# Kernel optimization log

Measured on AMD Instinct MI355X. Metric: run time of the kernel, lower is better.

## Reference

```python
import jax, jax.numpy as jnp
import numpy as np

B, D_IN, D_OUT, E = 8192, 1024, 1024, 16


def setup_inputs() -> dict:
    key = jax.random.key(0)
    k1, k2, k3 = jax.random.split(key, 3)
    x = jax.random.normal(k1, (B, D_IN), dtype=jnp.float32)
    Wg = jax.random.normal(k2, (D_IN, E), dtype=jnp.float32) * (1.0 / np.sqrt(D_IN))
    bg = jnp.zeros((E,), dtype=jnp.float32)
    We = jax.random.normal(k3, (E, D_IN, D_OUT), dtype=jnp.float32) * (1.0 / np.sqrt(D_IN))
    be = jnp.zeros((E, D_OUT), dtype=jnp.float32)
    return {"x": x, "Wg": Wg, "bg": bg, "We": We, "be": be}


def reference(x, Wg, bg, We, be):
    # Gate: [B, E]
    gate_out = x @ Wg + bg
    top1 = jnp.argmax(gate_out, axis=1)  # [B]
    # All-expert dense compute (faithful to the naive HardMoE): [B, E, D_OUT]
    expert_outs = jnp.einsum('bd,edh->beh', x, We) + be[None, :, :]
    # Gather each row's argmax expert output: [B, D_OUT]
    out = jnp.take_along_axis(expert_outs, top1[:, None, None], axis=1)[:, 0, :]
    return out
```

## Files before the change

### kernel.cpp

```cpp
#include <hip/hip_runtime.h>

typedef unsigned short u16;
typedef __attribute__((ext_vector_type(8))) short short8;
typedef __attribute__((ext_vector_type(4))) float floatx4;

#define NB 8192
#define DK 1024
#define DN 1024
#define NE 16
#define TM 128
#define TN 128
#define BK 64
#define MAX_TILES 80
#define GTHR 4e-3f

#define GATE_BLOCKS 512
#define WET_BLOCKS  2048

__device__ __forceinline__ u16 f2bf(float f) {
    union { float f; unsigned int u; } v; v.f = f;
    unsigned int u = v.u;
    return (u16)((u + 0x7fffu + ((u >> 16) & 1u)) >> 16);
}

__device__ __forceinline__ float bf2f(u16 h) {
    union { unsigned int u; float f; } v; v.u = ((unsigned int)h) << 16;
    return v.f;
}

__device__ __forceinline__ void gld16(const void* g, void* l) {
    __builtin_amdgcn_global_load_lds(
        (const __attribute__((address_space(1))) unsigned int*)g,
        (__attribute__((address_space(3))) unsigned int*)l, 16, 0, 0);
}

__global__ __launch_bounds__(256, 4) void k_prep(const float* __restrict__ x,
                                                 const float* __restrict__ Wg,
                                                 const float* __restrict__ bg,
                                                 const float* __restrict__ We,
                                                 u16* __restrict__ xb,
                                                 u16* __restrict__ WeT,
                                                 int* __restrict__ cnt,
                                                 int* __restrict__ bucket,
                                                 int* __restrict__ fixcnt,
                                                 int* __restrict__ fixlist) {
    __shared__ float gred[4][16 * 17];

    const int tid = threadIdx.x;

    if (blockIdx.x < GATE_BLOCKS) {
        const int lane = tid & 63;
        const int w = tid >> 6;
        const int lr = lane & 15, q = lane >> 4;
        const int R0 = blockIdx.x * 16;
        const size_t xrow = (size_t)(R0 + lr) * DK;

        floatx4 acc = (floatx4)0.0f;

        for (int cc = 0; cc < 4; ++cc) {
            const int kc = w * 256 + cc * 64;
            #pragma unroll
            for (int kwin = 0; kwin < 2; ++kwin) {
                const int kb = kc + kwin * 32 + q * 8;
                const float* gp = &x[xrow + kb];
                float4 v0 = *(const float4*)gp;
                float4 v1 = *(const float4*)(gp + 4);
                float av[8] = { v0.x, v0.y, v0.z, v0.w, v1.x, v1.y, v1.z, v1.w };
                u16 ah[8], al[8];
                #pragma unroll
                for (int j = 0; j < 8; ++j) {
                    ah[j] = f2bf(av[j]);
                    al[j] = f2bf(av[j] - bf2f(ah[j]));
                }
                *(short8*)&xb[xrow + kb] = *(const short8*)ah;
                float wv[8];
                #pragma unroll
                for (int j = 0; j < 8; ++j)
                    wv[j] = Wg[(size_t)(kb + j) * NE + lr];
                u16 bh[8], bl[8];
                #pragma unroll
                for (int j = 0; j < 8; ++j) {
                    bh[j] = f2bf(wv[j]);
                    bl[j] = f2bf(wv[j] - bf2f(bh[j]));
                }
                const short8 ahv = *(const short8*)ah;
                const short8 alv = *(const short8*)al;
                const short8 bhv = *(const short8*)bh;
                const short8 blv = *(const short8*)bl;
                acc = __builtin_amdgcn_mfma_f32_16x16x32_bf16(ahv, bhv, acc, 0, 0, 0);
                acc = __builtin_amdgcn_mfma_f32_16x16x32_bf16(ahv, blv, acc, 0, 0, 0);
                acc = __builtin_amdgcn_mfma_f32_16x16x32_bf16(alv, bhv, acc, 0, 0, 0);
            }
        }

        #pragma unroll
        for (int rr = 0; rr < 4; ++rr)
            gred[w][(q * 4 + rr) * 17 + lr] = acc[rr];
        __syncthreads();

        if (tid < 16) {
            int row = R0 + tid;
            float g[16];
            #pragma unroll
            for (int e = 0; e < 16; ++e)
                g[e] = gred[0][tid * 17 + e] + gred[1][tid * 17 + e]
                     + gred[2][tid * 17 + e] + gred[3][tid * 17 + e] + bg[e];
            float best = g[0], second = -1e30f; int bi = 0;
            #pragma unroll
            for (int e = 1; e < 16; ++e) {
                if (g[e] > best) { second = best; best = g[e]; bi = e; }
                else if (g[e] > second) second = g[e];
            }
            if (best - second >= GTHR) {
                int pos = atomicAdd(&cnt[bi], 1);
                bucket[bi * NB + pos] = row;
            } else {
                int f = atomicAdd(fixcnt, 1);
                fixlist[f] = row;
            }
        }
    } else {
        const int bw = blockIdx.x - GATE_BLOCKS;
        const int w = tid >> 6;
        const int lane = tid & 63;
        const int task = bw * 4 + w;
        const int ngrp = task & 15;
        const int kg   = (task >> 4) & 31;
        const int e    = task >> 9;
        const int n    = ngrp * 64 + lane;
        const float* src = We + ((size_t)e * DK + (size_t)kg * 32) * DN + n;
        float av[32];
        #pragma unroll
        for (int i = 0; i < 32; ++i)
            av[i] = src[(size_t)i * DN];
        u16 pk[32];
        #pragma unroll
        for (int i = 0; i < 32; ++i)
            pk[i] = f2bf(av[i]);
        u16* dst = WeT + ((size_t)e * DN + n) * DK + kg * 32;
        #pragma unroll
        for (int g = 0; g < 4; ++g)
            *(short8*)&dst[g * 8] = *(const short8*)&pk[g * 8];
    }
}

__global__ __launch_bounds__(256) void k_fix(const float* __restrict__ x,
                                             const float* __restrict__ Wg,
                                             const float* __restrict__ bg,
                                             const int* __restrict__ fixcnt,
                                             const int* __restrict__ fixlist,
                                             int* __restrict__ cnt,
                                             int* __restrict__ bucket) {
    __shared__ double lred[4][16];
    const int tid = threadIdx.x;
    const int lane = tid & 63;
    const int w = tid >> 6;
    const int n = *fixcnt;
    for (int it = blockIdx.x; it < n; it += 256) {
        const int row = fixlist[it];
        float4 xv = *(const float4*)&x[(size_t)row * DK + tid * 4];
        const float* xf = (const float*)&xv;
        double acc[16];
        #pragma unroll
        for (int e = 0; e < 16; ++e) acc[e] = 0.0;
        #pragma unroll
        for (int j = 0; j < 4; ++j) {
            int k = tid * 4 + j;
            double xd = (double)xf[j];
            const float4* wr = (const float4*)&Wg[(size_t)k * NE];
            float4 w0 = wr[0], w1 = wr[1], w2 = wr[2], w3 = wr[3];
            acc[0]  += xd * (double)w0.x;  acc[1]  += xd * (double)w0.y;
            acc[2]  += xd * (double)w0.z;  acc[3]  += xd * (double)w0.w;
            acc[4]  += xd * (double)w1.x;  acc[5]  += xd * (double)w1.y;
            acc[6]  += xd * (double)w1.z;  acc[7]  += xd * (double)w1.w;
            acc[8]  += xd * (double)w2.x;  acc[9]  += xd * (double)w2.y;
            acc[10] += xd * (double)w2.z;  acc[11] += xd * (double)w2.w;
            acc[12] += xd * (double)w3.x;  acc[13] += xd * (double)w3.y;
            acc[14] += xd * (double)w3.z;  acc[15] += xd * (double)w3.w;
        }
        #pragma unroll
        for (int e = 0; e < 16; ++e) {
            double v = acc[e];
            #pragma unroll
            for (int off = 1; off < 64; off <<= 1)
                v += __shfl_xor(v, off);
            acc[e] = v;
        }
        if (lane == 0) {
            #pragma unroll
            for (int e = 0; e < 16; ++e) lred[w][e] = acc[e];
        }
        __syncthreads();
        if (tid == 0) {
            double best = -1e300; int bi = 0;
            #pragma unroll
            for (int e = 0; e < 16; ++e) {
                double g = lred[0][e] + lred[1][e] + lred[2][e] + lred[3][e]
                         + (double)bg[e];
                if (g > best) { best = g; bi = e; }
            }
            int pos = atomicAdd(&cnt[bi], 1);
            bucket[bi * NB + pos] = row;
        }
        __syncthreads();
    }
}

__global__ __launch_bounds__(256) void k_moe(const u16* __restrict__ xb,
                                             const u16* __restrict__ WeT,
                                             const float* __restrict__ be,
                                             const int* __restrict__ bucket,
                                             const int* __restrict__ cnt,
                                             float* __restrict__ out) {
    const int slot = blockIdx.x >> 3;
    const int nt = blockIdx.x & 7;

    int e = -1, mt = 0, cntE = 0, acc_t = 0;
    #pragma unroll
    for (int ee = 0; ee < NE; ++ee) {
        int ce = cnt[ee];
        int nte = (ce + TM - 1) / TM;
        if (e < 0 && slot < acc_t + nte) { e = ee; mt = slot - acc_t; cntE = ce; }
        acc_t += nte;
    }
    if (e < 0) return;

    const int m0 = mt * TM;
    const int n0 = nt * TN;

    __shared__ u16 aLds[TM * BK];
    __shared__ u16 bLds[TN * BK];

    const int tid = threadIdx.x;
    const int lane = tid & 63;
    const int w = tid >> 6;
    const int wr = w >> 1, wc = w & 1;
    const int lr = lane & 15, q = lane >> 4;

    long aoff[4]; long boff[4]; int ldsb[4];
    #pragma unroll
    for (int r = 0; r < 4; ++r) {
        int c = r * 256 + tid;
        int row = c >> 3;
        int k16 = (c & 7) ^ (row & 7);
        int m_idx = m0 + row; if (m_idx >= cntE) m_idx = cntE - 1;
        long rid = bucket[e * NB + m_idx];
        aoff[r] = rid * DK + k16 * 8;
        boff[r] = (long)e * DN * DK + (long)(n0 + row) * DK + k16 * 8;
        ldsb[r] = (r * 256 + (tid & ~63)) * 8;
    }

    floatx4 acc[4][4];
    #pragma unroll
    for (int mi = 0; mi < 4; ++mi)
        #pragma unroll
        for (int ni = 0; ni < 4; ++ni)
            acc[mi][ni] = (floatx4)0.0f;

    for (int kk = 0; kk < DK; kk += BK) {
        #pragma unroll
        for (int r = 0; r < 4; ++r)
            gld16(xb + aoff[r] + kk, &aLds[ldsb[r]]);
        #pragma unroll
        for (int r = 0; r < 4; ++r)
            gld16(WeT + boff[r] + kk, &bLds[ldsb[r]]);
        __syncthreads();
        #pragma unroll
        for (int kwin = 0; kwin < 2; ++kwin) {
            const int sl = kwin * 4 + q;
            short8 af[4], bfr[4];
            #pragma unroll
            for (int mi = 0; mi < 4; ++mi) {
                int row = wr * 64 + mi * 16 + lr;
                af[mi] = *(const short8*)&aLds[row * BK + ((sl ^ (row & 7)) * 8)];
                int nrow = wc * 64 + mi * 16 + lr;
                bfr[mi] = *(const short8*)&bLds[nrow * BK + ((sl ^ (nrow & 7)) * 8)];
            }
            #pragma unroll
            for (int mi = 0; mi < 4; ++mi)
                #pragma unroll
                for (int ni = 0; ni < 4; ++ni)
                    acc[mi][ni] = __builtin_amdgcn_mfma_f32_16x16x32_bf16(
                        af[mi], bfr[ni], acc[mi][ni], 0, 0, 0);
        }
        __syncthreads();
    }

    float bias[4];
    #pragma unroll
    for (int ni = 0; ni < 4; ++ni)
        bias[ni] = be[e * DN + n0 + wc * 64 + ni * 16 + lr];

    #pragma unroll
    for (int mi = 0; mi < 4; ++mi) {
        #pragma unroll
        for (int rr = 0; rr < 4; ++rr) {
            int row_l = wr * 64 + mi * 16 + q * 4 + rr;
            int m_idx = m0 + row_l;
            if (m_idx < cntE) {
                long rid = bucket[e * NB + m_idx];
                float* orow = out + rid * DN + n0 + wc * 64 + lr;
                #pragma unroll
                for (int ni = 0; ni < 4; ++ni)
                    orow[ni * 16] = acc[mi][ni][rr] + bias[ni];
            }
        }
    }
}

extern "C" void kernel_launch(void* const* d_in, const int* in_sizes, int n_in,
                              void* d_out, int out_size, void* d_ws, size_t ws_size,
                              hipStream_t stream) {
    const float* x  = (const float*)d_in[0];
    const float* Wg = (const float*)d_in[1];
    const float* bg = (const float*)d_in[2];
    const float* We = (const float*)d_in[3];
    const float* be = (const float*)d_in[4];
    float* out = (float*)d_out;

    int* cnt     = (int*)d_ws;
    int* fixcnt  = cnt + 16;
    int* fixlist = cnt + 32;
    int* bucket  = cnt + 8448;
    u16* xb  = (u16*)((char*)d_ws + (1u << 20));
    u16* wet = (u16*)((char*)d_ws + (18u << 20));

    hipMemsetAsync(cnt, 0, 20 * sizeof(int), stream);
    k_prep<<<GATE_BLOCKS + WET_BLOCKS, 256, 0, stream>>>(x, Wg, bg, We, xb, wet,
                                                         cnt, bucket, fixcnt, fixlist);
    k_fix<<<256, 256, 0, stream>>>(x, Wg, bg, fixcnt, fixlist, cnt, bucket);
    k_moe<<<MAX_TILES * 8, 256, 0, stream>>>(xb, wet, be, bucket, cnt, out);
}
```

Measured before the change: 220.0 us.

## Split gate and weight-transpose into separate kernels and swizzle MoE block order

The fused prep kernel is split into a gate kernel and a transpose kernel. The transpose kernel gets its own higher occupancy bound and processes 16 rows at a time to cut register pressure. The MoE GEMM block index is remapped so consecutive blocks fall on different slots, which changes L2 reuse and load balance across CUs. The split adds one extra kernel launch and removes overlap between the gate and transpose work.

```diff
diff --git a/kernel.cpp b/kernel.cpp
--- a/kernel.cpp
+++ b/kernel.cpp
@@ -15,7 +15,7 @@
 #define GTHR 4e-3f
 
 #define GATE_BLOCKS 512
-#define WET_BLOCKS  2048
+#define TRANS_BLOCKS 2048
 
 __device__ __forceinline__ u16 f2bf(float f) {
     union { float f; unsigned int u; } v; v.f = f;
@@ -34,113 +34,113 @@
         (__attribute__((address_space(3))) unsigned int*)l, 16, 0, 0);
 }
 
-__global__ __launch_bounds__(256, 4) void k_prep(const float* __restrict__ x,
-                                                 const float* __restrict__ Wg,
-                                                 const float* __restrict__ bg,
-                                                 const float* __restrict__ We,
-                                                 u16* __restrict__ xb,
-                                                 u16* __restrict__ WeT,
-                                                 int* __restrict__ cnt,
-                                                 int* __restrict__ bucket,
-                                                 int* __restrict__ fixcnt,
-                                                 int* __restrict__ fixlist) {
+__global__ __launch_bounds__(256) void k_gate(const float* __restrict__ x,
+                                              const float* __restrict__ Wg,
+                                              const float* __restrict__ bg,
+                                              u16* __restrict__ xb,
+                                              int* __restrict__ cnt,
+                                              int* __restrict__ bucket,
+                                              int* __restrict__ fixcnt,
+                                              int* __restrict__ fixlist) {
     __shared__ float gred[4][16 * 17];
 
     const int tid = threadIdx.x;
-
-    if (blockIdx.x < GATE_BLOCKS) {
-        const int lane = tid & 63;
-        const int w = tid >> 6;
-        const int lr = lane & 15, q = lane >> 4;
-        const int R0 = blockIdx.x * 16;
-        const size_t xrow = (size_t)(R0 + lr) * DK;
-
-        floatx4 acc = (floatx4)0.0f;
-
-        for (int cc = 0; cc < 4; ++cc) {
-            const int kc = w * 256 + cc * 64;
-            #pragma unroll
-            for (int kwin = 0; kwin < 2; ++kwin) {
-                const int kb = kc + kwin * 32 + q * 8;
-                const float* gp = &x[xrow + kb];
-                float4 v0 = *(const float4*)gp;
-                float4 v1 = *(const float4*)(gp + 4);
-                float av[8] = { v0.x, v0.y, v0.z, v0.w, v1.x, v1.y, v1.z, v1.w };
-                u16 ah[8], al[8];
-                #pragma unroll
-                for (int j = 0; j < 8; ++j) {
-                    ah[j] = f2bf(av[j]);
-                    al[j] = f2bf(av[j] - bf2f(ah[j]));
-                }
-                *(short8*)&xb[xrow + kb] = *(const short8*)ah;
-                float wv[8];
-                #pragma unroll
-                for (int j = 0; j < 8; ++j)
-                    wv[j] = Wg[(size_t)(kb + j) * NE + lr];
-                u16 bh[8], bl[8];
-                #pragma unroll
-                for (int j = 0; j < 8; ++j) {
-                    bh[j] = f2bf(wv[j]);
-                    bl[j] = f2bf(wv[j] - bf2f(bh[j]));
-                }
-                const short8 ahv = *(const short8*)ah;
-                const short8 alv = *(const short8*)al;
-                const short8 bhv = *(const short8*)bh;
-                const short8 blv = *(const short8*)bl;
-                acc = __builtin_amdgcn_mfma_f32_16x16x32_bf16(ahv, bhv, acc, 0, 0, 0);
-                acc = __builtin_amdgcn_mfma_f32_16x16x32_bf16(ahv, blv, acc, 0, 0, 0);
-                acc = __builtin_amdgcn_mfma_f32_16x16x32_bf16(alv, bhv, acc, 0, 0, 0);
-            }
-        }
-
-        #pragma unroll
-        for (int rr = 0; rr < 4; ++rr)
-            gred[w][(q * 4 + rr) * 17 + lr] = acc[rr];
-        __syncthreads();
-
-        if (tid < 16) {
-            int row = R0 + tid;
-            float g[16];
-            #pragma unroll
-            for (int e = 0; e < 16; ++e)
-                g[e] = gred[0][tid * 17 + e] + gred[1][tid * 17 + e]
-                     + gred[2][tid * 17 + e] + gred[3][tid * 17 + e] + bg[e];
-            float best = g[0], second = -1e30f; int bi = 0;
-            #pragma unroll
-            for (int e = 1; e < 16; ++e) {
-                if (g[e] > best) { second = best; best = g[e]; bi = e; }
-                else if (g[e] > second) second = g[e];
-            }
-            if (best - second >= GTHR) {
-                int pos = atomicAdd(&cnt[bi], 1);
-                bucket[bi * NB + pos] = row;
-            } else {
-                int f = atomicAdd(fixcnt, 1);
-                fixlist[f] = row;
-            }
-        }
-    } else {
-        const int bw = blockIdx.x - GATE_BLOCKS;
-        const int w = tid >> 6;
-        const int lane = tid & 63;
-        const int task = bw * 4 + w;
-        const int ngrp = task & 15;
-        const int kg   = (task >> 4) & 31;
-        const int e    = task >> 9;
-        const int n    = ngrp * 64 + lane;
-        const float* src = We + ((size_t)e * DK + (size_t)kg * 32) * DN + n;
-        float av[32];
-        #pragma unroll
-        for (int i = 0; i < 32; ++i)
-            av[i] = src[(size_t)i * DN];
-        u16 pk[32];
-        #pragma unroll
-        for (int i = 0; i < 32; ++i)
+    const int lane = tid & 63;
+    const int w = tid >> 6;
+    const int lr = lane & 15, q = lane >> 4;
+    const int R0 = blockIdx.x * 16;
+    const size_t xrow = (size_t)(R0 + lr) * DK;
+
+    floatx4 acc = (floatx4)0.0f;
+
+    for (int cc = 0; cc < 4; ++cc) {
+        const int kc = w * 256 + cc * 64;
+        #pragma unroll
+        for (int kwin = 0; kwin < 2; ++kwin) {
+            const int kb = kc + kwin * 32 + q * 8;
+            const float* gp = &x[xrow + kb];
+            float4 v0 = *(const float4*)gp;
+            float4 v1 = *(const float4*)(gp + 4);
+            float av[8] = { v0.x, v0.y, v0.z, v0.w, v1.x, v1.y, v1.z, v1.w };
+            u16 ah[8], al[8];
+            #pragma unroll
+            for (int j = 0; j < 8; ++j) {
+                ah[j] = f2bf(av[j]);
+                al[j] = f2bf(av[j] - bf2f(ah[j]));
+            }
+            *(short8*)&xb[xrow + kb] = *(const short8*)ah;
+            float wv[8];
+            #pragma unroll
+            for (int j = 0; j < 8; ++j)
+                wv[j] = Wg[(size_t)(kb + j) * NE + lr];
+            u16 bh[8], bl[8];
+            #pragma unroll
+            for (int j = 0; j < 8; ++j) {
+                bh[j] = f2bf(wv[j]);
+                bl[j] = f2bf(wv[j] - bf2f(bh[j]));
+            }
+            const short8 ahv = *(const short8*)ah;
+            const short8 alv = *(const short8*)al;
+            const short8 bhv = *(const short8*)bh;
+            const short8 blv = *(const short8*)bl;
+            acc = __builtin_amdgcn_mfma_f32_16x16x32_bf16(ahv, bhv, acc, 0, 0, 0);
+            acc = __builtin_amdgcn_mfma_f32_16x16x32_bf16(ahv, blv, acc, 0, 0, 0);
+            acc = __builtin_amdgcn_mfma_f32_16x16x32_bf16(alv, bhv, acc, 0, 0, 0);
+        }
+    }
+
+    #pragma unroll
+    for (int rr = 0; rr < 4; ++rr)
+        gred[w][(q * 4 + rr) * 17 + lr] = acc[rr];
+    __syncthreads();
+
+    if (tid < 16) {
+        int row = R0 + tid;
+        float g[16];
+        #pragma unroll
+        for (int e = 0; e < 16; ++e)
+            g[e] = gred[0][tid * 17 + e] + gred[1][tid * 17 + e]
+                 + gred[2][tid * 17 + e] + gred[3][tid * 17 + e] + bg[e];
+        float best = g[0], second = -1e30f; int bi = 0;
+        #pragma unroll
+        for (int e = 1; e < 16; ++e) {
+            if (g[e] > best) { second = best; best = g[e]; bi = e; }
+            else if (g[e] > second) second = g[e];
+        }
+        if (best - second >= GTHR) {
+            int pos = atomicAdd(&cnt[bi], 1);
+            bucket[bi * NB + pos] = row;
+        } else {
+            int f = atomicAdd(fixcnt, 1);
+            fixlist[f] = row;
+        }
+    }
+}
+
+__global__ __launch_bounds__(256, 8) void k_trans(const float* __restrict__ We,
+                                                  u16* __restrict__ WeT) {
+    const int tid = threadIdx.x;
+    const int w = tid >> 6;
+    const int lane = tid & 63;
+    const int task = blockIdx.x * 4 + w;
+    const int ngrp = task & 15;
+    const int kg   = (task >> 4) & 31;
+    const int e    = task >> 9;
+    const int n    = ngrp * 64 + lane;
+    const float* src = We + ((size_t)e * DK + (size_t)kg * 32) * DN + n;
+    u16* dst = WeT + ((size_t)e * DN + n) * DK + kg * 32;
+    #pragma unroll
+    for (int h = 0; h < 2; ++h) {
+        float av[16];
+        #pragma unroll
+        for (int i = 0; i < 16; ++i)
+            av[i] = src[(size_t)(h * 16 + i) * DN];
+        u16 pk[16];
+        #pragma unroll
+        for (int i = 0; i < 16; ++i)
             pk[i] = f2bf(av[i]);
-        u16* dst = WeT + ((size_t)e * DN + n) * DK + kg * 32;
-        #pragma unroll
-        for (int g = 0; g < 4; ++g)
-            *(short8*)&dst[g * 8] = *(const short8*)&pk[g * 8];
+        *(short8*)&dst[h * 16 + 0] = *(const short8*)&pk[0];
+        *(short8*)&dst[h * 16 + 8] = *(const short8*)&pk[8];
     }
 }
 
@@ -212,8 +212,10 @@
                                              const int* __restrict__ bucket,
                                              const int* __restrict__ cnt,
                                              float* __restrict__ out) {
-    const int slot = blockIdx.x >> 3;
-    const int nt = blockIdx.x & 7;
+    const int bid = blockIdx.x;
+    const int swz = (bid & 7) * (MAX_TILES * 8 / 8) + (bid >> 3);
+    const int slot = swz >> 3;
+    const int nt = swz & 7;
 
     int e = -1, mt = 0, cntE = 0, acc_t = 0;
     #pragma unroll
@@ -326,8 +328,8 @@
     u16* wet = (u16*)((char*)d_ws + (18u << 20));
 
     hipMemsetAsync(cnt, 0, 20 * sizeof(int), stream);
-    k_prep<<<GATE_BLOCKS + WET_BLOCKS, 256, 0, stream>>>(x, Wg, bg, We, xb, wet,
-                                                         cnt, bucket, fixcnt, fixlist);
+    k_gate<<<GATE_BLOCKS, 256, 0, stream>>>(x, Wg, bg, xb, cnt, bucket, fixcnt, fixlist);
+    k_trans<<<TRANS_BLOCKS, 256, 0, stream>>>(We, wet);
     k_fix<<<256, 256, 0, stream>>>(x, Wg, bg, fixcnt, fixlist, cnt, bucket);
     k_moe<<<MAX_TILES * 8, 256, 0, stream>>>(xb, wet, be, bucket, cnt, out);
 }
```

New measurement: 240.2 us. 1.09x slower.

## Double-buffer LDS tiles in the MoE GEMM and swizzle the block order

Applied to the files above, without the earlier changes.

The expert GEMM kernel now keeps two LDS buffers for the A and B tiles. It prefetches the next K-slice with global_load_lds while MFMAs run on the current one, so global-load latency can overlap compute instead of stalling behind a barrier each iteration. The block index is also remapped with a swizzle, which changes which (tile, n-slice) pairs run together and so changes L2 reuse patterns. The cost is twice the LDS per block, which may lower occupancy. The new block ordering may help or hurt cache locality. A macro is also renamed.

```diff
diff --git a/kernel.cpp b/kernel.cpp
--- a/kernel.cpp
+++ b/kernel.cpp
@@ -15,7 +15,7 @@
 #define GTHR 4e-3f
 
 #define GATE_BLOCKS 512
-#define WET_BLOCKS  2048
+#define TRANS_BLOCKS 2048
 
 __device__ __forceinline__ u16 f2bf(float f) {
     union { float f; unsigned int u; } v; v.f = f;
@@ -212,8 +212,10 @@
                                              const int* __restrict__ bucket,
                                              const int* __restrict__ cnt,
                                              float* __restrict__ out) {
-    const int slot = blockIdx.x >> 3;
-    const int nt = blockIdx.x & 7;
+    const int bid = blockIdx.x;
+    const int swz = (bid & 7) * (MAX_TILES * 8 / 8) + (bid >> 3);
+    const int slot = swz >> 3;
+    const int nt = swz & 7;
 
     int e = -1, mt = 0, cntE = 0, acc_t = 0;
     #pragma unroll
@@ -228,8 +230,8 @@
     const int m0 = mt * TM;
     const int n0 = nt * TN;
 
-    __shared__ u16 aLds[TM * BK];
-    __shared__ u16 bLds[TN * BK];
+    __shared__ u16 aLds[2][TM * BK];
+    __shared__ u16 bLds[2][TN * BK];
 
     const int tid = threadIdx.x;
     const int lane = tid & 63;
@@ -257,14 +259,25 @@
         for (int ni = 0; ni < 4; ++ni)
             acc[mi][ni] = (floatx4)0.0f;
 
-    for (int kk = 0; kk < DK; kk += BK) {
-        #pragma unroll
-        for (int r = 0; r < 4; ++r)
-            gld16(xb + aoff[r] + kk, &aLds[ldsb[r]]);
-        #pragma unroll
-        for (int r = 0; r < 4; ++r)
-            gld16(WeT + boff[r] + kk, &bLds[ldsb[r]]);
-        __syncthreads();
+    #pragma unroll
+    for (int r = 0; r < 4; ++r)
+        gld16(xb + aoff[r], &aLds[0][ldsb[r]]);
+    #pragma unroll
+    for (int r = 0; r < 4; ++r)
+        gld16(WeT + boff[r], &bLds[0][ldsb[r]]);
+    __syncthreads();
+
+    int cur = 0;
+    for (int t = 0; t < DK / BK; ++t) {
+        if (t < DK / BK - 1) {
+            const long kk = (long)(t + 1) * BK;
+            #pragma unroll
+            for (int r = 0; r < 4; ++r)
+                gld16(xb + aoff[r] + kk, &aLds[cur ^ 1][ldsb[r]]);
+            #pragma unroll
+            for (int r = 0; r < 4; ++r)
+                gld16(WeT + boff[r] + kk, &bLds[cur ^ 1][ldsb[r]]);
+        }
         #pragma unroll
         for (int kwin = 0; kwin < 2; ++kwin) {
             const int sl = kwin * 4 + q;
@@ -272,9 +285,9 @@
             #pragma unroll
             for (int mi = 0; mi < 4; ++mi) {
                 int row = wr * 64 + mi * 16 + lr;
-                af[mi] = *(const short8*)&aLds[row * BK + ((sl ^ (row & 7)) * 8)];
+                af[mi] = *(const short8*)&aLds[cur][row * BK + ((sl ^ (row & 7)) * 8)];
                 int nrow = wc * 64 + mi * 16 + lr;
-                bfr[mi] = *(const short8*)&bLds[nrow * BK + ((sl ^ (nrow & 7)) * 8)];
+                bfr[mi] = *(const short8*)&bLds[cur][nrow * BK + ((sl ^ (nrow & 7)) * 8)];
             }
             #pragma unroll
             for (int mi = 0; mi < 4; ++mi)
@@ -284,6 +297,7 @@
                         af[mi], bfr[ni], acc[mi][ni], 0, 0, 0);
         }
         __syncthreads();
+        cur ^= 1;
     }
 
     float bias[4];
@@ -326,8 +340,8 @@
     u16* wet = (u16*)((char*)d_ws + (18u << 20));
 
     hipMemsetAsync(cnt, 0, 20 * sizeof(int), stream);
-    k_prep<<<GATE_BLOCKS + WET_BLOCKS, 256, 0, stream>>>(x, Wg, bg, We, xb, wet,
-                                                         cnt, bucket, fixcnt, fixlist);
+    k_prep<<<GATE_BLOCKS + TRANS_BLOCKS, 256, 0, stream>>>(x, Wg, bg, We, xb, wet,
+                                                           cnt, bucket, fixcnt, fixlist);
     k_fix<<<256, 256, 0, stream>>>(x, Wg, bg, fixcnt, fixlist, cnt, bucket);
     k_moe<<<MAX_TILES * 8, 256, 0, stream>>>(xb, wet, be, bucket, cnt, out);
 }
```

After: 225.9 us. 2.7% more time.
